# Optimization experiments

Measured on AMD Instinct MI355X. Metric: run time of the kernel, lower is better.

Reference implementation:

```python
import jax, jax.numpy as jnp
import numpy as np

B, S, D, H, FF = 1, 4096, 512, 8, 2048
DK = D // H
EPS = 1e-6


def layer_norm(x, alpha, beta):
    # Original LayerNorm: scalar alpha/beta, torch.std (ddof=1), eps added to std.
    mean = jnp.mean(x, axis=-1, keepdims=True)
    var = jnp.var(x, axis=-1, keepdims=True) * (D / (D - 1))  # Bessel-corrected, like torch.std
    std = jnp.sqrt(var)
    return alpha * (x - mean) / (std + EPS) + beta


def setup_inputs() -> dict:
    key = jax.random.key(0)
    ks = jax.random.split(key, 12)
    sd = 1.0 / np.sqrt(D)
    sf = 1.0 / np.sqrt(FF)
    inp = {
        "x": jax.random.normal(ks[0], (B, S, D), jnp.float32),
        "mask": jnp.ones((1, 1, 1, S), jnp.int32),
        "wq": jax.random.uniform(ks[1], (D, D), jnp.float32, -sd, sd),
        "bq": jnp.zeros((D,), jnp.float32),
        "wk": jax.random.uniform(ks[2], (D, D), jnp.float32, -sd, sd),
        "bk": jnp.zeros((D,), jnp.float32),
        "wv": jax.random.uniform(ks[3], (D, D), jnp.float32, -sd, sd),
        "bv": jnp.zeros((D,), jnp.float32),
        "wo": jax.random.uniform(ks[4], (D, D), jnp.float32, -sd, sd),
        "bo": jnp.zeros((D,), jnp.float32),
        "w1": jax.random.uniform(ks[5], (D, FF), jnp.float32, -sd, sd),
        "b1": jnp.zeros((FF,), jnp.float32),
        "w2": jax.random.uniform(ks[6], (FF, D), jnp.float32, -sf, sf),
        "b2": jnp.zeros((D,), jnp.float32),
        "ln1_a": jnp.ones((1,), jnp.float32),
        "ln1_b": jnp.zeros((1,), jnp.float32),
        "ln2_a": jnp.ones((1,), jnp.float32),
        "ln2_b": jnp.zeros((1,), jnp.float32),
    }
    return inp


def reference(x, mask, wq, bq, wk, bk, wv, bv, wo, bo, w1, b1, w2, b2,
              ln1_a, ln1_b, ln2_a, ln2_b):
    # --- pre-LN self-attention sublayer with residual ---
    h = layer_norm(x, ln1_a, ln1_b)
    q = (h @ wq + bq).reshape(B, S, H, DK).transpose(0, 2, 1, 3)  # [B,H,S,dk]
    k = (h @ wk + bk).reshape(B, S, H, DK).transpose(0, 2, 1, 3)
    v = (h @ wv + bv).reshape(B, S, H, DK).transpose(0, 2, 1, 3)
    scores = jnp.einsum('bhqd,bhkd->bhqk', q, k) / np.sqrt(DK)     # [B,H,S,S]
    scores = jnp.where(mask == 0, jnp.float32(-1e9), scores)
    probs = jax.nn.softmax(scores, axis=-1)
    attn = jnp.einsum('bhqk,bhkd->bhqd', probs, v)                 # [B,H,S,dk]
    attn = attn.transpose(0, 2, 1, 3).reshape(B, S, D)
    x = x + (attn @ wo + bo)
    # --- pre-LN feed-forward sublayer with residual ---
    h2 = layer_norm(x, ln2_a, ln2_b)
    ff = jax.nn.relu(h2 @ w1 + b1) @ w2 + b2
    return x + ff
```

## Files before the change

kernel.cpp:

```cpp
#include <hip/hip_runtime.h>
#include <hip/hip_bf16.h>

#define S_LEN 4096
#define D_DIM 512
#define H_NUM 8
#define DK_DIM 64
#define FF_DIM 2048
#define QLD 1536

typedef __attribute__((ext_vector_type(8))) short short8;
typedef __attribute__((ext_vector_type(4))) float f32x4;
typedef __attribute__((ext_vector_type(4))) ushort us4;

#if __has_builtin(__builtin_amdgcn_exp2f)
#define EXP2F __builtin_amdgcn_exp2f
#else
#define EXP2F exp2f
#endif

__device__ __forceinline__ ushort f2bf(float f) {
    union { float f; uint u; } v; v.f = f;
    uint r = v.u + 0x7FFF + ((v.u >> 16) & 1);
    return (ushort)(r >> 16);
}

__device__ __forceinline__ void gload_lds16(const void* g, void* l) {
    __builtin_amdgcn_global_load_lds(
        (const __attribute__((address_space(1))) void*)g,
        (__attribute__((address_space(3))) void*)l,
        16, 0, 0);
}

#define MFMA16(a, b, c) __builtin_amdgcn_mfma_f32_16x16x32_bf16(a, b, c, 0, 0, 0)

__global__ __launch_bounds__(256) void prep_all(
    const float* __restrict__ wq, const float* __restrict__ wk,
    const float* __restrict__ wv, const float* __restrict__ wo,
    const float* __restrict__ w1, const float* __restrict__ w2,
    const float* __restrict__ bq, const float* __restrict__ bk,
    const float* __restrict__ bv, const int* __restrict__ mask,
    ushort* __restrict__ wqkvt, ushort* __restrict__ wot,
    ushort* __restrict__ w1t, ushort* __restrict__ w2t,
    float* __restrict__ bqkv, float* __restrict__ mbias)
{
    __shared__ float t[32][33];
    const int bid = blockIdx.x, tid = threadIdx.x;
    if (bid < 3072) {
        const float* src; ushort* dst; int K, N, tx, ty;
        if (bid < 1024) {
            int wsel = bid >> 8, id = bid & 255;
            src = wsel == 0 ? wq : wsel == 1 ? wk : wsel == 2 ? wv : wo;
            dst = wsel == 0 ? wqkvt : wsel == 1 ? wqkvt + 512 * 512
                : wsel == 2 ? wqkvt + 1024 * 512 : wot;
            K = 512; N = 512; tx = id & 15; ty = id >> 4;
        } else if (bid < 2048) {
            int id = bid - 1024; src = w1; dst = w1t;
            K = 512; N = 2048; tx = id & 63; ty = id >> 6;
        } else {
            int id = bid - 2048; src = w2; dst = w2t;
            K = 2048; N = 512; tx = id & 15; ty = id >> 4;
        }
        int gn = tx * 32, gk = ty * 32;
        int lx = tid & 31, ly = tid >> 5;
#pragma unroll
        for (int i = 0; i < 32; i += 8)
            t[ly + i][lx] = src[(size_t)(gk + ly + i) * N + gn + lx];
        __syncthreads();
#pragma unroll
        for (int i = 0; i < 32; i += 8)
            dst[(size_t)(gn + ly + i) * K + gk + lx] = f2bf(t[lx][ly + i]);
    } else {
        int i = (bid - 3072) * 256 + tid;
        if (i < 512)       bqkv[i] = bq[i];
        else if (i < 1024) bqkv[i] = bk[i - 512];
        else if (i < 1536) bqkv[i] = bv[i - 1024];
        mbias[i] = mask[i] ? 0.0f : -1e9f;
    }
}

__global__ __launch_bounds__(256) void ln1_kernel(
    const float* __restrict__ x,
    const float* __restrict__ aP, const float* __restrict__ bP,
    ushort* __restrict__ out)
{
    const int row = blockIdx.x;
    const int d = threadIdx.x * 2;
    float2 v = *(const float2*)(x + (size_t)row * D_DIM + d);
    float sum = v.x + v.y;
    float sq  = v.x * v.x + v.y * v.y;
#pragma unroll
    for (int off = 1; off < 64; off <<= 1) {
        sum += __shfl_xor(sum, off);
        sq  += __shfl_xor(sq, off);
    }
    __shared__ float ssum[4], ssq[4];
    int wid = threadIdx.x >> 6;
    if ((threadIdx.x & 63) == 0) { ssum[wid] = sum; ssq[wid] = sq; }
    __syncthreads();
    sum = ssum[0] + ssum[1] + ssum[2] + ssum[3];
    sq  = ssq[0] + ssq[1] + ssq[2] + ssq[3];
    float mean = sum * (1.0f / D_DIM);
    float var  = (sq - (float)D_DIM * mean * mean) * (1.0f / (D_DIM - 1));
    var = fmaxf(var, 0.0f);
    float scale = aP[0] / (sqrtf(var) + 1e-6f);
    float beta  = bP[0];
    ushort2 o;
    o.x = f2bf((v.x - mean) * scale + beta);
    o.y = f2bf((v.y - mean) * scale + beta);
    *(ushort2*)(out + (size_t)row * D_DIM + d) = o;
}

__global__ __launch_bounds__(256) void ln2_fused(
    const float* __restrict__ x, const float* __restrict__ bo,
    const float* __restrict__ p0, const float* __restrict__ p1,
    const float* __restrict__ aP, const float* __restrict__ bP,
    float* __restrict__ x2, ushort* __restrict__ h2)
{
    const int row = blockIdx.x;
    const int d = threadIdx.x * 2;
    const size_t idx = (size_t)row * D_DIM + d;
    float2 xv = *(const float2*)(x + idx);
    float2 a0 = *(const float2*)(p0 + idx);
    float2 a1 = *(const float2*)(p1 + idx);
    float2 bb = *(const float2*)(bo + d);
    float2 v;
    v.x = xv.x + a0.x + a1.x + bb.x;
    v.y = xv.y + a0.y + a1.y + bb.y;
    *(float2*)(x2 + idx) = v;
    float sum = v.x + v.y;
    float sq  = v.x * v.x + v.y * v.y;
#pragma unroll
    for (int off = 1; off < 64; off <<= 1) {
        sum += __shfl_xor(sum, off);
        sq  += __shfl_xor(sq, off);
    }
    __shared__ float ssum[4], ssq[4];
    int wid = threadIdx.x >> 6;
    if ((threadIdx.x & 63) == 0) { ssum[wid] = sum; ssq[wid] = sq; }
    __syncthreads();
    sum = ssum[0] + ssum[1] + ssum[2] + ssum[3];
    sq  = ssq[0] + ssq[1] + ssq[2] + ssq[3];
    float mean = sum * (1.0f / D_DIM);
    float var  = (sq - (float)D_DIM * mean * mean) * (1.0f / (D_DIM - 1));
    var = fmaxf(var, 0.0f);
    float scale = aP[0] / (sqrtf(var) + 1e-6f);
    float beta  = bP[0];
    ushort2 o;
    o.x = f2bf((v.x - mean) * scale + beta);
    o.y = f2bf((v.y - mean) * scale + beta);
    *(ushort2*)(h2 + idx) = o;
}

__global__ __launch_bounds__(256) void gemm_mfma128(
    const ushort* __restrict__ A, const ushort* __restrict__ Bt,
    const float* __restrict__ bias,
    ushort* __restrict__ outB, ushort* __restrict__ outVT,
    int M, int N, int K, int relu)
{
    __shared__ union {
        struct { ushort As[2][128][32]; ushort Bs[2][128][32]; } s;
        ushort Es[4][32][68];
    } u;
    const int tid = threadIdx.x;
    const int w = tid >> 6, lane = tid & 63;
    const int l15 = lane & 15, quad = lane >> 4;
    const int wm = w >> 1, wn = w & 1;
    const int sw = (l15 >> 1) & 3;
    const int swc = ((lane & 3) ^ ((lane >> 3) & 3)) * 16;
    const int m0 = blockIdx.y * 128, n0 = blockIdx.x * 128;

    f32x4 acc[4][4] = {};

    const char* gA  = (const char*)(A  + (size_t)(m0 + 32 * w + (lane >> 2)) * K) + swc;
    const char* gA2 = gA + (size_t)16 * K * 2;
    const char* gB  = (const char*)(Bt + (size_t)(n0 + 32 * w + (lane >> 2)) * K) + swc;
    const char* gB2 = gB + (size_t)16 * K * 2;

    short8 ra[4], rb[4];
    auto preload = [&]() {
        ra[0] = *(const short8*)gA;        ra[1] = *(const short8*)gA2;
        ra[2] = *(const short8*)(gA + 64); ra[3] = *(const short8*)(gA2 + 64);
        rb[0] = *(const short8*)gB;        rb[1] = *(const short8*)gB2;
        rb[2] = *(const short8*)(gB + 64); rb[3] = *(const short8*)(gB2 + 64);
        gA += 128; gA2 += 128; gB += 128; gB2 += 128;
    };

    preload();
    const int nit = K >> 6;
    for (int t = 0; t < nit; ++t) {
        *(short8*)(&u.s.As[0][32 * w][0]      + lane * 8) = ra[0];
        *(short8*)(&u.s.As[0][32 * w + 16][0] + lane * 8) = ra[1];
        *(short8*)(&u.s.As[1][32 * w][0]      + lane * 8) = ra[2];
        *(short8*)(&u.s.As[1][32 * w + 16][0] + lane * 8) = ra[3];
        *(short8*)(&u.s.Bs[0][32 * w][0]      + lane * 8) = rb[0];
        *(short8*)(&u.s.Bs[0][32 * w + 16][0] + lane * 8) = rb[1];
        *(short8*)(&u.s.Bs[1][32 * w][0]      + lane * 8) = rb[2];
        *(short8*)(&u.s.Bs[1][32 * w + 16][0] + lane * 8) = rb[3];
        __syncthreads();
        if (t + 1 < nit) preload();
#pragma unroll
        for (int ks = 0; ks < 2; ++ks) {
            short8 af[4], bf[4];
#pragma unroll
            for (int i = 0; i < 4; ++i) {
                af[i] = *(const short8*)&u.s.As[ks][64 * wm + i * 16 + l15][(quad ^ sw) * 8];
                bf[i] = *(const short8*)&u.s.Bs[ks][64 * wn + i * 16 + l15][(quad ^ sw) * 8];
            }
#pragma unroll
            for (int mt = 0; mt < 4; ++mt)
#pragma unroll
                for (int nt = 0; nt < 4; ++nt)
                    acc[mt][nt] = MFMA16(af[mt], bf[nt], acc[mt][nt]);
        }
        __syncthreads();
    }

    if (outVT && n0 >= 1024) {
#pragma unroll
        for (int mt = 0; mt < 4; ++mt)
#pragma unroll
            for (int nt = 0; nt < 4; ++nt) {
                int nn = n0 + 64 * wn + nt * 16 + l15;
                int mmb = m0 + 64 * wm + mt * 16 + quad * 4;
                us4 pk;
#pragma unroll
                for (int r = 0; r < 4; ++r)
                    pk[r] = (short)f2bf(acc[mt][nt][r] + bias[nn]);
                *(us4*)(outVT + (size_t)(nn - 1024) * S_LEN + mmb) = pk;
            }
        return;
    }

#pragma unroll
    for (int h = 0; h < 2; ++h) {
#pragma unroll
        for (int mt = 2 * h; mt < 2 * h + 2; ++mt)
#pragma unroll
            for (int nt = 0; nt < 4; ++nt)
#pragma unroll
                for (int r = 0; r < 4; ++r) {
                    float v = acc[mt][nt][r] + bias[n0 + 64 * wn + nt * 16 + l15];
                    if (relu) v = fmaxf(v, 0.0f);
                    u.Es[w][(mt & 1) * 16 + quad * 4 + r][nt * 16 + l15] = f2bf(v);
                }
        __syncthreads();
#pragma unroll
        for (int p2 = 0; p2 < 4; ++p2) {
            int row = p2 * 8 + (lane >> 3);
            int col = (lane & 7) * 8;
            short8 vv = *(const short8*)&u.Es[w][row][col];
            *(short8*)(outB + (size_t)(m0 + 64 * wm + h * 32 + row) * N
                             + n0 + 64 * wn + col) = vv;
        }
        __syncthreads();
    }
}

__global__ __launch_bounds__(256) void gemm_mfma(
    const ushort* __restrict__ A, const ushort* __restrict__ Bt,
    float* __restrict__ outF,
    int M, int N, int K, int ksl)
{
    __shared__ ushort As[2][2][128][32];
    __shared__ ushort Bs[2][2][64][32];
    const int tid = threadIdx.x;
    const int w = tid >> 6, lane = tid & 63;
    const int l15 = lane & 15, quad = lane >> 4;
    const int sw = (l15 >> 1) & 3;
    const int swc = ((lane & 3) ^ ((lane >> 3) & 3)) * 16;
    const int m0 = blockIdx.y * 128, n0 = blockIdx.x * 64;
    const int kz = blockIdx.z;
    const int kbeg = kz * ksl;

    f32x4 acc[2][4] = {};

    const char* gA  = (const char*)(A  + (size_t)(m0 + 32 * w + (lane >> 2)) * K + kbeg) + swc;
    const char* gA2 = gA + (size_t)16 * K * 2;
    const char* gB  = (const char*)(Bt + (size_t)(n0 + 16 * w + (lane >> 2)) * K + kbeg) + swc;

    auto stage = [&](int b) {
        gload_lds16(gA,       &As[b][0][32 * w][0]);
        gload_lds16(gA + 64,  &As[b][1][32 * w][0]);
        gload_lds16(gA2,      &As[b][0][32 * w + 16][0]);
        gload_lds16(gA2 + 64, &As[b][1][32 * w + 16][0]);
        gload_lds16(gB,       &Bs[b][0][16 * w][0]);
        gload_lds16(gB + 64,  &Bs[b][1][16 * w][0]);
        gA += 128; gA2 += 128; gB += 128;
    };

    stage(0);
    const int nit = ksl >> 6;
    for (int t = 0; t < nit; ++t) {
        __syncthreads();
        if (t + 1 < nit) stage((t + 1) & 1);
        const int b = t & 1;
#pragma unroll
        for (int ks = 0; ks < 2; ++ks) {
            short8 a0 = *(const short8*)&As[b][ks][32 * w + l15][(quad ^ sw) * 8];
            short8 a1 = *(const short8*)&As[b][ks][32 * w + 16 + l15][(quad ^ sw) * 8];
            short8 b0 = *(const short8*)&Bs[b][ks][0 * 16 + l15][(quad ^ sw) * 8];
            short8 b1 = *(const short8*)&Bs[b][ks][1 * 16 + l15][(quad ^ sw) * 8];
            short8 b2 = *(const short8*)&Bs[b][ks][2 * 16 + l15][(quad ^ sw) * 8];
            short8 b3 = *(const short8*)&Bs[b][ks][3 * 16 + l15][(quad ^ sw) * 8];
            acc[0][0] = MFMA16(a0, b0, acc[0][0]);
            acc[0][1] = MFMA16(a0, b1, acc[0][1]);
            acc[0][2] = MFMA16(a0, b2, acc[0][2]);
            acc[0][3] = MFMA16(a0, b3, acc[0][3]);
            acc[1][0] = MFMA16(a1, b0, acc[1][0]);
            acc[1][1] = MFMA16(a1, b1, acc[1][1]);
            acc[1][2] = MFMA16(a1, b2, acc[1][2]);
            acc[1][3] = MFMA16(a1, b3, acc[1][3]);
        }
    }

    float* of = outF + (size_t)kz * M * N;
#pragma unroll
    for (int mt = 0; mt < 2; ++mt)
#pragma unroll
        for (int nt = 0; nt < 4; ++nt)
#pragma unroll
            for (int r = 0; r < 4; ++r) {
                int mm = m0 + 32 * w + mt * 16 + quad * 4 + r;
                int nn = n0 + nt * 16 + l15;
                of[(size_t)mm * N + nn] = acc[mt][nt][r];
            }
}

__global__ __launch_bounds__(256, 2) void flash_mfma(
    const ushort* __restrict__ qkv, const ushort* __restrict__ vbt,
    const float* __restrict__ mbias, ushort* __restrict__ at_bf)
{
    __shared__ ushort Ks[2][128][32];
    __shared__ ushort Vt[4][64][32];
    __shared__ ushort Pld[4][64][40];

    const int bid = blockIdx.x;
    const int head = bid & 7;
    const int q0 = (bid >> 3) * 64;
    const int tid = threadIdx.x;
    const int w = tid >> 6, lane = tid & 63;
    const int l15 = lane & 15, quad = lane >> 4;
    const int hoff = head * DK_DIM;
    const int sw = (l15 >> 1) & 3;
    const int swc = ((lane & 3) ^ ((lane >> 3) & 3)) * 16;

    short8 qf[2][4];
#pragma unroll
    for (int ks = 0; ks < 2; ++ks)
#pragma unroll
        for (int nt = 0; nt < 4; ++nt)
            qf[ks][nt] = *(const short8*)(qkv
                + (size_t)(q0 + nt * 16 + l15) * QLD + hoff + ks * 32 + quad * 8);

    const char* gk0 = (const char*)(qkv + (size_t)(32 * w + (lane >> 2)) * QLD + 512 + hoff) + swc;
    const char* gv0 = (const char*)(vbt + (size_t)(lane >> 2) * S_LEN + w * 32) + swc;

    short8 rk[4], rv[4];
    auto preload = [&](int ktg) {
        const char* gk = gk0 + (size_t)ktg * (QLD * 2);
        rk[0] = *(const short8*)gk;
        rk[1] = *(const short8*)(gk + (size_t)16 * QLD * 2);
        rk[2] = *(const short8*)(gk + 64);
        rk[3] = *(const short8*)(gk + (size_t)16 * QLD * 2 + 64);
        const char* gv = gv0 + ktg * 2;
        rv[0] = *(const short8*)gv;
        rv[1] = *(const short8*)(gv + (size_t)16 * S_LEN * 2);
        rv[2] = *(const short8*)(gv + (size_t)32 * S_LEN * 2);
        rv[3] = *(const short8*)(gv + (size_t)48 * S_LEN * 2);
    };
    preload(0);

    const short8 ones = {0x3F80, 0x3F80, 0x3F80, 0x3F80,
                         0x3F80, 0x3F80, 0x3F80, 0x3F80};
    f32x4 oacc[4][4] = {};
    f32x4 lacc[4] = {};

    const int NIT = S_LEN / 128;
    for (int t = 0; t < NIT; ++t) {
        *(short8*)(&Ks[0][32 * w][0]      + lane * 8) = rk[0];
        *(short8*)(&Ks[0][32 * w + 16][0] + lane * 8) = rk[1];
        *(short8*)(&Ks[1][32 * w][0]      + lane * 8) = rk[2];
        *(short8*)(&Ks[1][32 * w + 16][0] + lane * 8) = rk[3];
        *(short8*)(&Vt[w][0][0]  + lane * 8) = rv[0];
        *(short8*)(&Vt[w][16][0] + lane * 8) = rv[1];
        *(short8*)(&Vt[w][32][0] + lane * 8) = rv[2];
        *(short8*)(&Vt[w][48][0] + lane * 8) = rv[3];
        if (t + 1 < NIT) preload((t + 1) * 128);
        const int ktg = t * 128;

#pragma unroll
        for (int kh = 0; kh < 2; ++kh) {
            f32x4 sacc[4] = {};
#pragma unroll
            for (int ks = 0; ks < 2; ++ks) {
                short8 kf = *(const short8*)&Ks[ks][32 * w + kh * 16 + l15][(quad ^ sw) * 8];
#pragma unroll
                for (int nt = 0; nt < 4; ++nt)
                    sacc[nt] = MFMA16(kf, qf[ks][nt], sacc[nt]);
            }
            f32x4 mb = *(const f32x4*)&mbias[ktg + 32 * w + kh * 16 + quad * 4];
#pragma unroll
            for (int nt = 0; nt < 4; ++nt) {
                us4 pk;
#pragma unroll
                for (int r = 0; r < 4; ++r) {
                    float pv = EXP2F(fmaf(sacc[nt][r], 0.18033688011112042f, mb[r]));
                    pk[r] = (ushort)(__float_as_uint(pv) >> 16);
                }
                *(us4*)&Pld[w][nt * 16 + l15][kh * 16 + quad * 4] = pk;
            }
        }

        short8 bvr[4];
#pragma unroll
        for (int nt = 0; nt < 4; ++nt)
            bvr[nt] = *(const short8*)&Vt[w][nt * 16 + l15][(quad ^ sw) * 8];
#pragma unroll
        for (int mt = 0; mt < 4; ++mt) {
            short8 ap = *(const short8*)&Pld[w][mt * 16 + l15][quad * 8];
            lacc[mt] = MFMA16(ap, ones, lacc[mt]);
#pragma unroll
            for (int nt = 0; nt < 4; ++nt)
                oacc[mt][nt] = MFMA16(ap, bvr[nt], oacc[mt][nt]);
        }
    }

    __syncthreads();

    float* Ored = (float*)&Pld[0][0][0];
    float* lred = (float*)&Ks[0][0][0];
    const int qloc = tid >> 4, dk4 = (tid & 15) * 4;
    if (l15 == 0) {
#pragma unroll
        for (int m2 = 0; m2 < 4; ++m2)
#pragma unroll
            for (int r = 0; r < 4; ++r)
                lred[w * 64 + m2 * 16 + quad * 4 + r] = lacc[m2][r];
    }
#pragma unroll
    for (int mt = 0; mt < 4; ++mt) {
        if (mt) __syncthreads();
#pragma unroll
        for (int nt = 0; nt < 4; ++nt)
#pragma unroll
            for (int r = 0; r < 4; ++r)
                Ored[(w * 16 + quad * 4 + r) * 68 + nt * 16 + l15] = oacc[mt][nt][r];
        __syncthreads();
        f32x4 s = *(const f32x4*)&Ored[qloc * 68 + dk4];
#pragma unroll
        for (int ww = 1; ww < 4; ++ww)
            s += *(const f32x4*)&Ored[(ww * 16 + qloc) * 68 + dk4];
        float l = lred[mt * 16 + qloc] + lred[64 + mt * 16 + qloc]
                + lred[128 + mt * 16 + qloc] + lred[192 + mt * 16 + qloc];
        float inv = 1.0f / l;
        us4 pk;
#pragma unroll
        for (int j = 0; j < 4; ++j) pk[j] = (short)f2bf(s[j] * inv);
        *(us4*)&at_bf[(size_t)(q0 + mt * 16 + qloc) * D_DIM + hoff + dk4] = pk;
    }
}

__global__ __launch_bounds__(256) void ff2_combine(
    const float* __restrict__ x2, const float* __restrict__ b2,
    const float* __restrict__ p0, const float* __restrict__ p1,
    float* __restrict__ out)
{
    size_t i = ((size_t)blockIdx.x * 256 + threadIdx.x) * 4;
    f32x4 a  = *(const f32x4*)(x2 + i);
    f32x4 q0 = *(const f32x4*)(p0 + i);
    f32x4 q1 = *(const f32x4*)(p1 + i);
    f32x4 bb = *(const f32x4*)(b2 + (int)(i & 511));
    f32x4 r = a + q0 + q1 + bb;
    *(f32x4*)(out + i) = r;
}

extern "C" void kernel_launch(void* const* d_in, const int* in_sizes, int n_in,
                              void* d_out, int out_size, void* d_ws, size_t ws_size,
                              hipStream_t stream) {
    (void)in_sizes; (void)n_in; (void)out_size; (void)ws_size;
    const float* x    = (const float*)d_in[0];
    const int*   mask = (const int*)d_in[1];
    const float* wq = (const float*)d_in[2];
    const float* bq = (const float*)d_in[3];
    const float* wk = (const float*)d_in[4];
    const float* bk = (const float*)d_in[5];
    const float* wv = (const float*)d_in[6];
    const float* bv = (const float*)d_in[7];
    const float* wo = (const float*)d_in[8];
    const float* bo = (const float*)d_in[9];
    const float* w1 = (const float*)d_in[10];
    const float* b1 = (const float*)d_in[11];
    const float* w2 = (const float*)d_in[12];
    const float* b2 = (const float*)d_in[13];
    const float* ln1a = (const float*)d_in[14];
    const float* ln1b = (const float*)d_in[15];
    const float* ln2a = (const float*)d_in[16];
    const float* ln2b = (const float*)d_in[17];
    float* out = (float*)d_out;

    const size_t SD = (size_t)S_LEN * D_DIM;
    char* p = (char*)d_ws;
    ushort* wqkvt = (ushort*)p; p += (size_t)1536 * 512 * 2;
    ushort* wot   = (ushort*)p; p += (size_t)512 * 512 * 2;
    ushort* w1t   = (ushort*)p; p += (size_t)2048 * 512 * 2;
    ushort* w2t   = (ushort*)p; p += (size_t)512 * 2048 * 2;
    float*  bqkv  = (float*)p;  p += 1536 * 4;
    float*  mbias = (float*)p;  p += 4096 * 4;
    ushort* h_bf  = (ushort*)p; p += SD * 2;
    ushort* qkv   = (ushort*)p; p += (size_t)4096 * 1536 * 2;
    ushort* vbt   = (ushort*)p; p += SD * 2;
    ushort* at_bf = (ushort*)p; p += SD * 2;
    float*  x2    = (float*)p;  p += SD * 4;
    ushort* h2    = (ushort*)p; p += SD * 2;
    ushort* ff1   = (ushort*)p; p += (size_t)4096 * 2048 * 2;
    float* wopart  = (float*)h_bf;
    float* ff2part = (float*)h_bf;

    dim3 blk(256);

    prep_all<<<dim3(3088), blk, 0, stream>>>(wq, wk, wv, wo, w1, w2, bq, bk, bv,
                                             mask, wqkvt, wot, w1t, w2t, bqkv, mbias);

    ln1_kernel<<<dim3(S_LEN), blk, 0, stream>>>(x, ln1a, ln1b, h_bf);

    gemm_mfma128<<<dim3(12, 32), blk, 0, stream>>>(
        h_bf, wqkvt, bqkv, qkv, vbt, S_LEN, 1536, 512, 0);

    flash_mfma<<<dim3(512), blk, 0, stream>>>(qkv, vbt, mbias, at_bf);

    gemm_mfma<<<dim3(8, 32, 2), blk, 0, stream>>>(
        at_bf, wot, wopart, S_LEN, 512, 512, 256);

    ln2_fused<<<dim3(S_LEN), blk, 0, stream>>>(x, bo, wopart, wopart + SD,
                                               ln2a, ln2b, x2, h2);

    gemm_mfma128<<<dim3(16, 32), blk, 0, stream>>>(
        h2, w1t, b1, ff1, nullptr, S_LEN, 2048, 512, 1);

    gemm_mfma<<<dim3(8, 32, 2), blk, 0, stream>>>(
        ff1, w2t, ff2part, S_LEN, 512, 2048, 1024);

    ff2_combine<<<dim3(2048), blk, 0, stream>>>(
        x2, b2, ff2part, ff2part + SD, out);
}
```

Measured before the change: 227.9 us.

## Split attention over two KV halves, read K directly, merge LN1 into prep

The flash attention kernel now splits the key/value range into two halves across a second grid dimension, doubling the block count. Each half writes unnormalized fp32 partial outputs and row sums, which a new combine kernel adds and normalizes into bf16. K fragments are now loaded straight from global memory instead of being staged through LDS, and the LN1 kernel is merged into the weight-prep launch to save one launch. The combine works without max rescaling because softmax here has no running max, and in exchange it adds an extra pass over fp32 partials plus more global K traffic.

```diff
diff --git a/kernel.cpp b/kernel.cpp
--- a/kernel.cpp
+++ b/kernel.cpp
@@ -33,7 +33,7 @@
 
 #define MFMA16(a, b, c) __builtin_amdgcn_mfma_f32_16x16x32_bf16(a, b, c, 0, 0, 0)
 
-__global__ __launch_bounds__(256) void prep_all(
+__global__ __launch_bounds__(256) void prep_ln(
     const float* __restrict__ wq, const float* __restrict__ wk,
     const float* __restrict__ wv, const float* __restrict__ wo,
     const float* __restrict__ w1, const float* __restrict__ w2,
@@ -41,9 +41,13 @@
     const float* __restrict__ bv, const int* __restrict__ mask,
     ushort* __restrict__ wqkvt, ushort* __restrict__ wot,
     ushort* __restrict__ w1t, ushort* __restrict__ w2t,
-    float* __restrict__ bqkv, float* __restrict__ mbias)
+    float* __restrict__ bqkv, float* __restrict__ mbias,
+    const float* __restrict__ x,
+    const float* __restrict__ aP, const float* __restrict__ bP,
+    ushort* __restrict__ h_bf)
 {
     __shared__ float t[32][33];
+    __shared__ float ssum[4], ssq[4];
     const int bid = blockIdx.x, tid = threadIdx.x;
     if (bid < 3072) {
         const float* src; ushort* dst; int K, N, tx, ty;
@@ -69,45 +73,38 @@
 #pragma unroll
         for (int i = 0; i < 32; i += 8)
             dst[(size_t)(gn + ly + i) * K + gk + lx] = f2bf(t[lx][ly + i]);
-    } else {
+    } else if (bid < 3088) {
         int i = (bid - 3072) * 256 + tid;
         if (i < 512)       bqkv[i] = bq[i];
         else if (i < 1024) bqkv[i] = bk[i - 512];
         else if (i < 1536) bqkv[i] = bv[i - 1024];
         mbias[i] = mask[i] ? 0.0f : -1e9f;
-    }
-}
-
-__global__ __launch_bounds__(256) void ln1_kernel(
-    const float* __restrict__ x,
-    const float* __restrict__ aP, const float* __restrict__ bP,
-    ushort* __restrict__ out)
-{
-    const int row = blockIdx.x;
-    const int d = threadIdx.x * 2;
-    float2 v = *(const float2*)(x + (size_t)row * D_DIM + d);
-    float sum = v.x + v.y;
-    float sq  = v.x * v.x + v.y * v.y;
-#pragma unroll
-    for (int off = 1; off < 64; off <<= 1) {
-        sum += __shfl_xor(sum, off);
-        sq  += __shfl_xor(sq, off);
-    }
-    __shared__ float ssum[4], ssq[4];
-    int wid = threadIdx.x >> 6;
-    if ((threadIdx.x & 63) == 0) { ssum[wid] = sum; ssq[wid] = sq; }
-    __syncthreads();
-    sum = ssum[0] + ssum[1] + ssum[2] + ssum[3];
-    sq  = ssq[0] + ssq[1] + ssq[2] + ssq[3];
-    float mean = sum * (1.0f / D_DIM);
-    float var  = (sq - (float)D_DIM * mean * mean) * (1.0f / (D_DIM - 1));
-    var = fmaxf(var, 0.0f);
-    float scale = aP[0] / (sqrtf(var) + 1e-6f);
-    float beta  = bP[0];
-    ushort2 o;
-    o.x = f2bf((v.x - mean) * scale + beta);
-    o.y = f2bf((v.y - mean) * scale + beta);
-    *(ushort2*)(out + (size_t)row * D_DIM + d) = o;
+    } else {
+        const int row = bid - 3088;
+        const int d = tid * 2;
+        float2 v = *(const float2*)(x + (size_t)row * D_DIM + d);
+        float sum = v.x + v.y;
+        float sq  = v.x * v.x + v.y * v.y;
+#pragma unroll
+        for (int off = 1; off < 64; off <<= 1) {
+            sum += __shfl_xor(sum, off);
+            sq  += __shfl_xor(sq, off);
+        }
+        int wid = tid >> 6;
+        if ((tid & 63) == 0) { ssum[wid] = sum; ssq[wid] = sq; }
+        __syncthreads();
+        sum = ssum[0] + ssum[1] + ssum[2] + ssum[3];
+        sq  = ssq[0] + ssq[1] + ssq[2] + ssq[3];
+        float mean = sum * (1.0f / D_DIM);
+        float var  = (sq - (float)D_DIM * mean * mean) * (1.0f / (D_DIM - 1));
+        var = fmaxf(var, 0.0f);
+        float scale = aP[0] / (sqrtf(var) + 1e-6f);
+        float beta  = bP[0];
+        ushort2 o;
+        o.x = f2bf((v.x - mean) * scale + beta);
+        o.y = f2bf((v.y - mean) * scale + beta);
+        *(ushort2*)(h_bf + (size_t)row * D_DIM + d) = o;
+    }
 }
 
 __global__ __launch_bounds__(256) void ln2_fused(
@@ -328,15 +325,18 @@
 
 __global__ __launch_bounds__(256, 2) void flash_mfma(
     const ushort* __restrict__ qkv, const ushort* __restrict__ vbt,
-    const float* __restrict__ mbias, ushort* __restrict__ at_bf)
-{
-    __shared__ ushort Ks[2][128][32];
+    const float* __restrict__ mbias,
+    float* __restrict__ pO, float* __restrict__ pl)
+{
     __shared__ ushort Vt[4][64][32];
     __shared__ ushort Pld[4][64][40];
-
-    const int bid = blockIdx.x;
-    const int head = bid & 7;
-    const int q0 = (bid >> 3) * 64;
+    __shared__ float lred[256];
+
+    const int bx = blockIdx.x;
+    const int head = bx & 7;
+    const int q0 = (bx >> 3) * 64;
+    const int half = blockIdx.y;
+    const int kvbeg = half * (S_LEN / 2);
     const int tid = threadIdx.x;
     const int w = tid >> 6, lane = tid & 63;
     const int l15 = lane & 15, quad = lane >> 4;
@@ -352,53 +352,45 @@
             qf[ks][nt] = *(const short8*)(qkv
                 + (size_t)(q0 + nt * 16 + l15) * QLD + hoff + ks * 32 + quad * 8);
 
-    const char* gk0 = (const char*)(qkv + (size_t)(32 * w + (lane >> 2)) * QLD + 512 + hoff) + swc;
-    const char* gv0 = (const char*)(vbt + (size_t)(lane >> 2) * S_LEN + w * 32) + swc;
-
-    short8 rk[4], rv[4];
-    auto preload = [&](int ktg) {
-        const char* gk = gk0 + (size_t)ktg * (QLD * 2);
-        rk[0] = *(const short8*)gk;
-        rk[1] = *(const short8*)(gk + (size_t)16 * QLD * 2);
-        rk[2] = *(const short8*)(gk + 64);
-        rk[3] = *(const short8*)(gk + (size_t)16 * QLD * 2 + 64);
+    const ushort* kb = qkv + (size_t)(kvbeg + 32 * w + l15) * QLD + 512 + hoff + quad * 8;
+    const char* gv0 = (const char*)(vbt + (size_t)(lane >> 2) * S_LEN + kvbeg + w * 32) + swc;
+
+    short8 rv[4];
+    auto preloadV = [&](int ktg) {
         const char* gv = gv0 + ktg * 2;
         rv[0] = *(const short8*)gv;
         rv[1] = *(const short8*)(gv + (size_t)16 * S_LEN * 2);
         rv[2] = *(const short8*)(gv + (size_t)32 * S_LEN * 2);
         rv[3] = *(const short8*)(gv + (size_t)48 * S_LEN * 2);
     };
-    preload(0);
+    preloadV(0);
 
     const short8 ones = {0x3F80, 0x3F80, 0x3F80, 0x3F80,
                          0x3F80, 0x3F80, 0x3F80, 0x3F80};
     f32x4 oacc[4][4] = {};
     f32x4 lacc[4] = {};
 
-    const int NIT = S_LEN / 128;
+    const int NIT = (S_LEN / 2) / 128;
     for (int t = 0; t < NIT; ++t) {
-        *(short8*)(&Ks[0][32 * w][0]      + lane * 8) = rk[0];
-        *(short8*)(&Ks[0][32 * w + 16][0] + lane * 8) = rk[1];
-        *(short8*)(&Ks[1][32 * w][0]      + lane * 8) = rk[2];
-        *(short8*)(&Ks[1][32 * w + 16][0] + lane * 8) = rk[3];
+        const int ktg = t * 128;
         *(short8*)(&Vt[w][0][0]  + lane * 8) = rv[0];
         *(short8*)(&Vt[w][16][0] + lane * 8) = rv[1];
         *(short8*)(&Vt[w][32][0] + lane * 8) = rv[2];
         *(short8*)(&Vt[w][48][0] + lane * 8) = rv[3];
-        if (t + 1 < NIT) preload((t + 1) * 128);
-        const int ktg = t * 128;
+        if (t + 1 < NIT) preloadV((t + 1) * 128);
 
 #pragma unroll
         for (int kh = 0; kh < 2; ++kh) {
+            const ushort* kp = kb + (size_t)(ktg + kh * 16) * QLD;
+            short8 kf0 = *(const short8*)kp;
+            short8 kf1 = *(const short8*)(kp + 32);
             f32x4 sacc[4] = {};
 #pragma unroll
-            for (int ks = 0; ks < 2; ++ks) {
-                short8 kf = *(const short8*)&Ks[ks][32 * w + kh * 16 + l15][(quad ^ sw) * 8];
-#pragma unroll
-                for (int nt = 0; nt < 4; ++nt)
-                    sacc[nt] = MFMA16(kf, qf[ks][nt], sacc[nt]);
+            for (int nt = 0; nt < 4; ++nt) {
+                sacc[nt] = MFMA16(kf0, qf[0][nt], sacc[nt]);
+                sacc[nt] = MFMA16(kf1, qf[1][nt], sacc[nt]);
             }
-            f32x4 mb = *(const f32x4*)&mbias[ktg + 32 * w + kh * 16 + quad * 4];
+            f32x4 mb = *(const f32x4*)&mbias[kvbeg + ktg + 32 * w + kh * 16 + quad * 4];
 #pragma unroll
             for (int nt = 0; nt < 4; ++nt) {
                 us4 pk;
@@ -428,7 +420,6 @@
     __syncthreads();
 
     float* Ored = (float*)&Pld[0][0][0];
-    float* lred = (float*)&Ks[0][0][0];
     const int qloc = tid >> 4, dk4 = (tid & 15) * 4;
     if (l15 == 0) {
 #pragma unroll
@@ -437,6 +428,7 @@
             for (int r = 0; r < 4; ++r)
                 lred[w * 64 + m2 * 16 + quad * 4 + r] = lacc[m2][r];
     }
+    float* pOh = pO + (size_t)half * S_LEN * D_DIM;
 #pragma unroll
     for (int mt = 0; mt < 4; ++mt) {
         if (mt) __syncthreads();
@@ -450,14 +442,31 @@
 #pragma unroll
         for (int ww = 1; ww < 4; ++ww)
             s += *(const f32x4*)&Ored[(ww * 16 + qloc) * 68 + dk4];
-        float l = lred[mt * 16 + qloc] + lred[64 + mt * 16 + qloc]
-                + lred[128 + mt * 16 + qloc] + lred[192 + mt * 16 + qloc];
-        float inv = 1.0f / l;
-        us4 pk;
-#pragma unroll
-        for (int j = 0; j < 4; ++j) pk[j] = (short)f2bf(s[j] * inv);
-        *(us4*)&at_bf[(size_t)(q0 + mt * 16 + qloc) * D_DIM + hoff + dk4] = pk;
-    }
+        *(f32x4*)&pOh[(size_t)(q0 + mt * 16 + qloc) * D_DIM + hoff + dk4] = s;
+        if (dk4 == 0) {
+            float l = lred[mt * 16 + qloc] + lred[64 + mt * 16 + qloc]
+                    + lred[128 + mt * 16 + qloc] + lred[192 + mt * 16 + qloc];
+            pl[((size_t)half * H_NUM + head) * S_LEN + q0 + mt * 16 + qloc] = l;
+        }
+    }
+}
+
+__global__ __launch_bounds__(256) void flash_comb(
+    const float* __restrict__ pO, const float* __restrict__ pl,
+    ushort* __restrict__ at_bf)
+{
+    const size_t SD = (size_t)S_LEN * D_DIM;
+    size_t i = ((size_t)blockIdx.x * 256 + threadIdx.x) * 4;
+    int s = (int)(i >> 9), d = (int)(i & 511), head = d >> 6;
+    float l = pl[(size_t)head * S_LEN + s] +
+              pl[((size_t)H_NUM + head) * S_LEN + s];
+    f32x4 a = *(const f32x4*)(pO + i);
+    f32x4 b = *(const f32x4*)(pO + SD + i);
+    float inv = 1.0f / l;
+    us4 pk;
+#pragma unroll
+    for (int j = 0; j < 4; ++j) pk[j] = (short)f2bf((a[j] + b[j]) * inv);
+    *(us4*)(at_bf + i) = pk;
 }
 
 __global__ __launch_bounds__(256) void ff2_combine(
@@ -506,6 +515,7 @@
     ushort* w2t   = (ushort*)p; p += (size_t)512 * 2048 * 2;
     float*  bqkv  = (float*)p;  p += 1536 * 4;
     float*  mbias = (float*)p;  p += 4096 * 4;
+    float*  pl    = (float*)p;  p += (size_t)2 * H_NUM * S_LEN * 4;
     ushort* h_bf  = (ushort*)p; p += SD * 2;
     ushort* qkv   = (ushort*)p; p += (size_t)4096 * 1536 * 2;
     ushort* vbt   = (ushort*)p; p += SD * 2;
@@ -513,20 +523,21 @@
     float*  x2    = (float*)p;  p += SD * 4;
     ushort* h2    = (ushort*)p; p += SD * 2;
     ushort* ff1   = (ushort*)p; p += (size_t)4096 * 2048 * 2;
+    float* pO      = (float*)ff1;
     float* wopart  = (float*)h_bf;
     float* ff2part = (float*)h_bf;
 
     dim3 blk(256);
 
-    prep_all<<<dim3(3088), blk, 0, stream>>>(wq, wk, wv, wo, w1, w2, bq, bk, bv,
-                                             mask, wqkvt, wot, w1t, w2t, bqkv, mbias);
-
-    ln1_kernel<<<dim3(S_LEN), blk, 0, stream>>>(x, ln1a, ln1b, h_bf);
+    prep_ln<<<dim3(7184), blk, 0, stream>>>(wq, wk, wv, wo, w1, w2, bq, bk, bv,
+                                            mask, wqkvt, wot, w1t, w2t, bqkv, mbias,
+                                            x, ln1a, ln1b, h_bf);
 
     gemm_mfma128<<<dim3(12, 32), blk, 0, stream>>>(
         h_bf, wqkvt, bqkv, qkv, vbt, S_LEN, 1536, 512, 0);
 
-    flash_mfma<<<dim3(512), blk, 0, stream>>>(qkv, vbt, mbias, at_bf);
+    flash_mfma<<<dim3(512, 2), blk, 0, stream>>>(qkv, vbt, mbias, pO, pl);
+    flash_comb<<<dim3(2048), blk, 0, stream>>>(pO, pl, at_bf);
 
     gemm_mfma<<<dim3(8, 32, 2), blk, 0, stream>>>(
         at_bf, wot, wopart, S_LEN, 512, 512, 256);
```

New measurement: 242.7 us. +6.5%, slower.
